# Performance work log

Measured on AMD Instinct MI355X. Metric: run time of the kernel, lower is better.

Reference implementation:

```python
import jax, jax.numpy as jnp
import numpy as np

B, S, H, DEPTH = 2, 2048, 8, 64
D_MODEL = H * DEPTH  # 512


def setup_inputs() -> dict:
    key = jax.random.key(0)
    ks = jax.random.split(key, 6)
    s = 0.02
    return {
        "emb_x": jax.random.normal(ks[0], (B, S, D_MODEL), dtype=jnp.float32),
        "pe_rel_t": jax.random.normal(ks[1], (B, S, D_MODEL), dtype=jnp.float32),
        "Wq": jax.random.normal(ks[2], (D_MODEL, D_MODEL), dtype=jnp.float32) * s,
        "bq": jnp.zeros((D_MODEL,), dtype=jnp.float32),
        "Wk": jax.random.normal(ks[3], (D_MODEL, D_MODEL), dtype=jnp.float32) * s,
        "bk": jnp.zeros((D_MODEL,), dtype=jnp.float32),
        "Wv": jax.random.normal(ks[4], (D_MODEL, D_MODEL), dtype=jnp.float32) * s,
        "bv": jnp.zeros((D_MODEL,), dtype=jnp.float32),
        "Wo": jax.random.normal(ks[5], (D_MODEL, D_MODEL), dtype=jnp.float32) * s,
        "bo": jnp.zeros((D_MODEL,), dtype=jnp.float32),
    }


def _split_heads(x):
    # [B, S, D_MODEL] -> [B, H, S, DEPTH]
    b, s, _ = x.shape
    return x.reshape(b, s, H, DEPTH).transpose(0, 2, 1, 3)


def reference(emb_x, pe_rel_t, Wq, bq, Wk, bk, Wv, bv, Wo, bo):
    # RPE attention: content and relative-position streams share WQ/WK.
    Q_c = _split_heads(emb_x @ Wq + bq)
    Q_r = _split_heads(pe_rel_t @ Wq + bq)
    K_c = _split_heads(emb_x @ Wk + bk)
    K_r = _split_heads(pe_rel_t @ Wk + bk)
    V_c = _split_heads(emb_x @ Wv + bv)

    logits = (
        jnp.einsum("bhqd,bhkd->bhqk", Q_c, K_c)
        + jnp.einsum("bhqd,bhkd->bhqk", Q_r, K_c)
        + jnp.einsum("bhqd,bhkd->bhqk", Q_c, K_r)
    ) / jnp.sqrt(jnp.asarray(DEPTH, dtype=emb_x.dtype))

    attn = jax.nn.softmax(logits, axis=-1)  # [B, H, S, S]
    z = jnp.einsum("bhqk,bhkd->bhqd", attn, V_c)  # [B, H, S, DEPTH]
    z = z.transpose(0, 2, 1, 3).reshape(emb_x.shape[0], -1, D_MODEL)
    out = z @ Wo + bo
    return out, attn
```

## Files before the change

### kernel.cpp

```cpp
#include <hip/hip_runtime.h>
#include <hip/hip_bf16.h>


typedef __bf16 bf16;
typedef bf16 bf16x4 __attribute__((ext_vector_type(4)));
typedef bf16 bf16x8 __attribute__((ext_vector_type(8)));
typedef float f32x4 __attribute__((ext_vector_type(4)));

#define B_ 2
#define S_ 2048
#define H_ 8
#define D_ 64
#define DM_ 512
#define M_ 4096

__global__ __launch_bounds__(256) void pack_x(const float4* __restrict__ emb,
                                              const float4* __restrict__ pe,
                                              bf16* __restrict__ xb,
                                              bf16* __restrict__ xp,
                                              bf16* __restrict__ xs) {
    int i = blockIdx.x * 256 + threadIdx.x;
    float4 a = emb[i], b = pe[i];
    int o = i * 4;
    bf16x4 va, vp, vs;
    va.x = (bf16)a.x; va.y = (bf16)a.y; va.z = (bf16)a.z; va.w = (bf16)a.w;
    vp.x = (bf16)b.x; vp.y = (bf16)b.y; vp.z = (bf16)b.z; vp.w = (bf16)b.w;
    vs.x = (bf16)(a.x + b.x); vs.y = (bf16)(a.y + b.y);
    vs.z = (bf16)(a.z + b.z); vs.w = (bf16)(a.w + b.w);
    *(bf16x4*)(xb + o) = va;
    *(bf16x4*)(xp + o) = vp;
    *(bf16x4*)(xs + o) = vs;
}

__global__ __launch_bounds__(256) void pack_w(const float* __restrict__ W,
                                              bf16* __restrict__ WT) {
    int idx = blockIdx.x * 256 + threadIdx.x;
    int n = idx >> 9, k = idx & 511;
    WT[idx] = (bf16)W[k * 512 + n];
}

template <int AMODE, int SMODE>
__global__ __launch_bounds__(256) void proj_gemm(const bf16* __restrict__ A,
                                                 const bf16* __restrict__ BT,
                                                 const float* __restrict__ bias,
                                                 float bscale,
                                                 void* __restrict__ Cout) {
    __shared__ bf16 As[64][72];
    __shared__ bf16 Bs[64][72];
    const int tid = threadIdx.x;
    const int lane = tid & 63;
    const int wave = tid >> 6;
    const int wm = wave >> 1, wn = wave & 1;
    const int row0 = blockIdx.x * 64;
    const int col0 = blockIdx.y * 64;
    const int lm = lane & 15, lk = (lane >> 4) * 8;

    f32x4 acc[2][2] = {{{0.f,0.f,0.f,0.f},{0.f,0.f,0.f,0.f}},
                       {{0.f,0.f,0.f,0.f},{0.f,0.f,0.f,0.f}}};

    for (int k0 = 0; k0 < 512; k0 += 64) {
        for (int i = 0; i < 2; ++i) {
            int idx = tid + i * 256;
            int r = idx >> 3, sg = (idx & 7) * 8;
            long aoff;
            int arow = row0 + r, acol = k0 + sg;
            if (AMODE == 0) {
                aoff = (long)arow * 512 + acol;
            } else {
                int b = arow >> 11, s = arow & 2047, h = acol >> 6, d = acol & 63;
                aoff = (((long)(b * H_ + h) * S_ + s) * 64) + d;
            }
            *(bf16x8*)&As[r][sg] = *(const bf16x8*)(A + aoff);
            *(bf16x8*)&Bs[r][sg] = *(const bf16x8*)(BT + (long)(col0 + r) * 512 + k0 + sg);
        }
        __syncthreads();
        for (int kk = 0; kk < 64; kk += 32) {
            bf16x8 af[2], bfr[2];
            for (int t = 0; t < 2; ++t) {
                af[t]  = *(const bf16x8*)&As[wm * 32 + t * 16 + lm][kk + lk];
                bfr[t] = *(const bf16x8*)&Bs[wn * 32 + t * 16 + lm][kk + lk];
            }
            for (int mt = 0; mt < 2; ++mt)
                for (int nt = 0; nt < 2; ++nt)
                    acc[mt][nt] = __builtin_amdgcn_mfma_f32_16x16x32_bf16(
                        af[mt], bfr[nt], acc[mt][nt], 0, 0, 0);
        }
        __syncthreads();
    }

    const int rbase = (lane >> 4) * 4;
    for (int mt = 0; mt < 2; ++mt)
        for (int nt = 0; nt < 2; ++nt)
            for (int r = 0; r < 4; ++r) {
                int row = row0 + wm * 32 + mt * 16 + rbase + r;
                int col = col0 + wn * 32 + nt * 16 + lm;
                float v = acc[mt][nt][r] + bias[col] * bscale;
                int b = row >> 11, s = row & 2047, h = col >> 6, d = col & 63;
                if (SMODE == 0) {
                    ((bf16*)Cout)[(((long)(b * H_ + h) * S_ + s) * 64) + d] = (bf16)v;
                } else if (SMODE == 1) {
                    ((bf16*)Cout)[(((long)(b * H_ + h) * 64 + d) * S_) + s] = (bf16)v;
                } else {
                    ((float*)Cout)[(long)row * 512 + col] = v;
                }
            }
}

__global__ __launch_bounds__(256) void attn_kernel(const bf16* __restrict__ Qc,
                                                   const bf16* __restrict__ Qr,
                                                   const bf16* __restrict__ Kc,
                                                   const bf16* __restrict__ Ks,
                                                   const bf16* __restrict__ Vt,
                                                   bf16* __restrict__ Zb,
                                                   float* __restrict__ attn_out) {
    __shared__ bf16 Kcs[64][72];
    __shared__ bf16 Kss[64][72];
    __shared__ bf16 Vts[64][72];
    __shared__ bf16 ptile[4][16][40];

    const int tid = threadIdx.x, lane = tid & 63, wave = tid >> 6;
    const int bh = blockIdx.x >> 5;
    const int qt = blockIdx.x & 31;
    const int qw = qt * 64 + wave * 16;
    const long kbase = (long)bh * (S_ * 64);
    const long vbase = (long)bh * (64 * S_);
    const int lm = lane & 15, lk = (lane >> 4) * 8;
    const float SC = 0.125f;

    bf16x8 qcf[2], qrf[2];
    for (int kt = 0; kt < 2; ++kt) {
        long off = kbase + (long)(qw + lm) * 64 + kt * 32 + lk;
        qcf[kt] = *(const bf16x8*)(Qc + off);
        qrf[kt] = *(const bf16x8*)(Qr + off);
    }

    float rsum[4] = {0.f, 0.f, 0.f, 0.f};
    f32x4 zacc[4] = {{0.f,0.f,0.f,0.f},{0.f,0.f,0.f,0.f},
                     {0.f,0.f,0.f,0.f},{0.f,0.f,0.f,0.f}};

    for (int key0 = 0; key0 < S_; key0 += 64) {
        __syncthreads();
        for (int i = 0; i < 2; ++i) {
            int idx = tid + i * 256, r = idx >> 3, sg = (idx & 7) * 8;
            *(bf16x8*)&Kcs[r][sg] = *(const bf16x8*)(Kc + kbase + (long)(key0 + r) * 64 + sg);
            *(bf16x8*)&Kss[r][sg] = *(const bf16x8*)(Ks + kbase + (long)(key0 + r) * 64 + sg);
            *(bf16x8*)&Vts[r][sg] = *(const bf16x8*)(Vt + vbase + (long)r * S_ + key0 + sg);
        }
        __syncthreads();
        for (int pair = 0; pair < 2; ++pair) {
            for (int nt = 0; nt < 2; ++nt) {
                const int keyl = pair * 32 + nt * 16;
                f32x4 acc = {0.f, 0.f, 0.f, 0.f};
                for (int kt = 0; kt < 2; ++kt) {
                    bf16x8 bs = *(const bf16x8*)&Kss[keyl + lm][kt * 32 + lk];
                    bf16x8 bc = *(const bf16x8*)&Kcs[keyl + lm][kt * 32 + lk];
                    acc = __builtin_amdgcn_mfma_f32_16x16x32_bf16(qcf[kt], bs, acc, 0, 0, 0);
                    acc = __builtin_amdgcn_mfma_f32_16x16x32_bf16(qrf[kt], bc, acc, 0, 0, 0);
                }
                for (int r = 0; r < 4; ++r) {
                    float p = __expf(acc[r] * SC);
                    rsum[r] += p;
                    ptile[wave][(lane >> 4) * 4 + r][nt * 16 + lm] = (bf16)p;
                }
            }
            __syncthreads();
            bf16x8 pa = *(const bf16x8*)&ptile[wave][lm][lk];
            for (int nt = 0; nt < 4; ++nt) {
                bf16x8 vb = *(const bf16x8*)&Vts[nt * 16 + lm][pair * 32 + lk];
                zacc[nt] = __builtin_amdgcn_mfma_f32_16x16x32_bf16(pa, vb, zacc[nt], 0, 0, 0);
            }
        }
    }

    float inv_r[4];
    for (int r = 0; r < 4; ++r) {
        float s = rsum[r];
        s += __shfl_xor(s, 1);
        s += __shfl_xor(s, 2);
        s += __shfl_xor(s, 4);
        s += __shfl_xor(s, 8);
        inv_r[r] = 1.0f / s;
    }

    for (int nt = 0; nt < 4; ++nt)
        for (int r = 0; r < 4; ++r)
            Zb[kbase + (long)(qw + (lane >> 4) * 4 + r) * 64 + nt * 16 + lm] =
                (bf16)(zacc[nt][r] * inv_r[r]);

    const long abase = (long)bh * S_ * S_;
    for (int key0 = 0; key0 < S_; key0 += 64) {
        __syncthreads();
        for (int i = 0; i < 2; ++i) {
            int idx = tid + i * 256, r = idx >> 3, sg = (idx & 7) * 8;
            *(bf16x8*)&Kcs[r][sg] = *(const bf16x8*)(Kc + kbase + (long)(key0 + r) * 64 + sg);
            *(bf16x8*)&Kss[r][sg] = *(const bf16x8*)(Ks + kbase + (long)(key0 + r) * 64 + sg);
        }
        __syncthreads();
        for (int nt = 0; nt < 4; ++nt) {
            const int keyl = nt * 16;
            f32x4 acc = {0.f, 0.f, 0.f, 0.f};
            for (int kt = 0; kt < 2; ++kt) {
                bf16x8 bs = *(const bf16x8*)&Kss[keyl + lm][kt * 32 + lk];
                bf16x8 bc = *(const bf16x8*)&Kcs[keyl + lm][kt * 32 + lk];
                acc = __builtin_amdgcn_mfma_f32_16x16x32_bf16(qcf[kt], bs, acc, 0, 0, 0);
                acc = __builtin_amdgcn_mfma_f32_16x16x32_bf16(qrf[kt], bc, acc, 0, 0, 0);
            }
            for (int r = 0; r < 4; ++r) {
                float p = __expf(acc[r] * SC) * inv_r[r];
                attn_out[abase + (long)(qw + (lane >> 4) * 4 + r) * S_ + key0 + keyl + lm] = p;
            }
        }
    }
}

extern "C" void kernel_launch(void* const* d_in, const int* in_sizes, int n_in,
                              void* d_out, int out_size, void* d_ws, size_t ws_size,
                              hipStream_t stream) {
    const float* emb = (const float*)d_in[0];
    const float* pe  = (const float*)d_in[1];
    const float* Wq  = (const float*)d_in[2];
    const float* bq  = (const float*)d_in[3];
    const float* Wk  = (const float*)d_in[4];
    const float* bk  = (const float*)d_in[5];
    const float* Wv  = (const float*)d_in[6];
    const float* bv  = (const float*)d_in[7];
    const float* Wo  = (const float*)d_in[8];
    const float* bo  = (const float*)d_in[9];

    float* outp = (float*)d_out;
    float* attn = outp + (long)B_ * S_ * DM_;

    char* w = (char*)d_ws;
    const long SZ_X = (long)M_ * DM_ * 2;
    const long SZ_W = (long)DM_ * DM_ * 2;
    bf16* Xb  = (bf16*)(w);
    bf16* Xp  = (bf16*)(w + SZ_X);
    bf16* Xs  = (bf16*)(w + 2 * SZ_X);
    bf16* WqT = (bf16*)(w + 3 * SZ_X);
    bf16* WkT = (bf16*)(w + 3 * SZ_X + SZ_W);
    bf16* WvT = (bf16*)(w + 3 * SZ_X + 2 * SZ_W);
    bf16* WoT = (bf16*)(w + 3 * SZ_X + 3 * SZ_W);
    char* p2  = w + 3 * SZ_X + 4 * SZ_W;
    bf16* Qc  = (bf16*)(p2);
    bf16* Qr  = (bf16*)(p2 + SZ_X);
    bf16* Kc  = (bf16*)(p2 + 2 * SZ_X);
    bf16* Ks  = (bf16*)(p2 + 3 * SZ_X);
    bf16* Vt  = (bf16*)(p2 + 4 * SZ_X);
    bf16* Zb  = (bf16*)(p2 + 5 * SZ_X);

    pack_x<<<(M_ * DM_ / 4) / 256, 256, 0, stream>>>(
        (const float4*)emb, (const float4*)pe, Xb, Xp, Xs);
    pack_w<<<(DM_ * DM_) / 256, 256, 0, stream>>>(Wq, WqT);
    pack_w<<<(DM_ * DM_) / 256, 256, 0, stream>>>(Wk, WkT);
    pack_w<<<(DM_ * DM_) / 256, 256, 0, stream>>>(Wv, WvT);
    pack_w<<<(DM_ * DM_) / 256, 256, 0, stream>>>(Wo, WoT);

    dim3 g(M_ / 64, DM_ / 64);
    proj_gemm<0, 0><<<g, 256, 0, stream>>>(Xb, WqT, bq, 1.f, Qc);
    proj_gemm<0, 0><<<g, 256, 0, stream>>>(Xp, WqT, bq, 1.f, Qr);
    proj_gemm<0, 0><<<g, 256, 0, stream>>>(Xb, WkT, bk, 1.f, Kc);
    proj_gemm<0, 0><<<g, 256, 0, stream>>>(Xs, WkT, bk, 2.f, Ks);
    proj_gemm<0, 1><<<g, 256, 0, stream>>>(Xb, WvT, bv, 1.f, Vt);

    attn_kernel<<<B_ * H_ * (S_ / 64), 256, 0, stream>>>(
        Qc, Qr, Kc, Ks, Vt, Zb, attn);

    proj_gemm<1, 2><<<g, 256, 0, stream>>>(Zb, WoT, bo, 1.f, (void*)outp);
}
```

Baseline: 429.9 us.

## Double-buffer attention K/V tiles, coalesce attn stores, batch weight packs and projections

The attention kernel now double-buffers Kc/Ks/Vt tiles in shared memory, prefetching the next tile into registers while computing the current one. It also removes the per-pair intra-block barrier and stores the fp32 attention matrix through an LDS staging buffer as float4 writes. The four weight transposes become one tiled kernel launch, and the five QKV projection GEMMs become one launch over a 40-column grid. Together these aim to cut global-memory latency stalls, uncoalesced writes of the large attention output, and launch overhead, at the cost of more shared memory and register pressure, which may reduce occupancy.

```diff
diff --git a/kernel.cpp b/kernel.cpp
--- a/kernel.cpp
+++ b/kernel.cpp
@@ -10,7 +10,6 @@
 #define B_ 2
 #define S_ 2048
 #define H_ 8
-#define D_ 64
 #define DM_ 512
 #define M_ 4096
 
@@ -32,24 +31,116 @@
     *(bf16x4*)(xs + o) = vs;
 }
 
-__global__ __launch_bounds__(256) void pack_w(const float* __restrict__ W,
-                                              bf16* __restrict__ WT) {
-    int idx = blockIdx.x * 256 + threadIdx.x;
-    int n = idx >> 9, k = idx & 511;
-    WT[idx] = (bf16)W[k * 512 + n];
-}
-
-template <int AMODE, int SMODE>
-__global__ __launch_bounds__(256) void proj_gemm(const bf16* __restrict__ A,
-                                                 const bf16* __restrict__ BT,
-                                                 const float* __restrict__ bias,
-                                                 float bscale,
-                                                 void* __restrict__ Cout) {
+__global__ __launch_bounds__(256) void pack_tw(
+    const float* __restrict__ W0, const float* __restrict__ W1,
+    const float* __restrict__ W2, const float* __restrict__ W3,
+    bf16* __restrict__ T0, bf16* __restrict__ T1,
+    bf16* __restrict__ T2, bf16* __restrict__ T3) {
+    __shared__ bf16 tile[64][66];
+    const float* W; bf16* T;
+    switch (blockIdx.z) {
+        case 0: W = W0; T = T0; break;
+        case 1: W = W1; T = T1; break;
+        case 2: W = W2; T = T2; break;
+        default: W = W3; T = T3; break;
+    }
+    const int tid = threadIdx.x;
+    const int r = tid >> 2, c = (tid & 3) * 16;
+    const int r0 = blockIdx.x * 64, c0 = blockIdx.y * 64;
+    for (int j = 0; j < 16; j += 4) {
+        float4 v = *(const float4*)&W[(long)(r0 + r) * 512 + c0 + c + j];
+        tile[r][c + j + 0] = (bf16)v.x; tile[r][c + j + 1] = (bf16)v.y;
+        tile[r][c + j + 2] = (bf16)v.z; tile[r][c + j + 3] = (bf16)v.w;
+    }
+    __syncthreads();
+    bf16x8 o0, o1;
+#pragma unroll
+    for (int j = 0; j < 8; ++j) { o0[j] = tile[c + j][r]; o1[j] = tile[c + 8 + j][r]; }
+    *(bf16x8*)&T[(long)(c0 + r) * 512 + r0 + c] = o0;
+    *(bf16x8*)&T[(long)(c0 + r) * 512 + r0 + c + 8] = o1;
+}
+
+__global__ __launch_bounds__(256) void proj5(
+    const bf16* __restrict__ Xb, const bf16* __restrict__ Xp, const bf16* __restrict__ Xs,
+    const bf16* __restrict__ WqT, const bf16* __restrict__ WkT, const bf16* __restrict__ WvT,
+    const float* __restrict__ bq, const float* __restrict__ bk, const float* __restrict__ bv,
+    bf16* __restrict__ Qc, bf16* __restrict__ Qr, bf16* __restrict__ Kc,
+    bf16* __restrict__ Ks, bf16* __restrict__ Vt) {
+    __shared__ bf16 As[64][72];
+    __shared__ bf16 Bs[64][72];
+    const int pj = blockIdx.y >> 3;
+    const int col0 = (blockIdx.y & 7) * 64;
+    const bf16* A; const bf16* BT; const float* bias; float bsc = 1.f;
+    bf16* out; int vmode = 0;
+    switch (pj) {
+        case 0: A = Xb; BT = WqT; bias = bq; out = Qc; break;
+        case 1: A = Xp; BT = WqT; bias = bq; out = Qr; break;
+        case 2: A = Xb; BT = WkT; bias = bk; out = Kc; break;
+        case 3: A = Xs; BT = WkT; bias = bk; bsc = 2.f; out = Ks; break;
+        default: A = Xb; BT = WvT; bias = bv; out = Vt; vmode = 1; break;
+    }
+    const int tid = threadIdx.x;
+    const int lane = tid & 63, wave = tid >> 6;
+    const int wm = wave >> 1, wn = wave & 1;
+    const int row0 = blockIdx.x * 64;
+    const int lm = lane & 15, lk = (lane >> 4) * 8;
+
+    f32x4 acc[2][2] = {{{0.f,0.f,0.f,0.f},{0.f,0.f,0.f,0.f}},
+                       {{0.f,0.f,0.f,0.f},{0.f,0.f,0.f,0.f}}};
+
+    for (int k0 = 0; k0 < 512; k0 += 64) {
+#pragma unroll
+        for (int i = 0; i < 2; ++i) {
+            int idx = tid + i * 256;
+            int r = idx >> 3, sg = (idx & 7) * 8;
+            *(bf16x8*)&As[r][sg] = *(const bf16x8*)(A + (long)(row0 + r) * 512 + k0 + sg);
+            *(bf16x8*)&Bs[r][sg] = *(const bf16x8*)(BT + (long)(col0 + r) * 512 + k0 + sg);
+        }
+        __syncthreads();
+#pragma unroll
+        for (int kk = 0; kk < 64; kk += 32) {
+            bf16x8 af[2], bfr[2];
+#pragma unroll
+            for (int t = 0; t < 2; ++t) {
+                af[t]  = *(const bf16x8*)&As[wm * 32 + t * 16 + lm][kk + lk];
+                bfr[t] = *(const bf16x8*)&Bs[wn * 32 + t * 16 + lm][kk + lk];
+            }
+#pragma unroll
+            for (int mt = 0; mt < 2; ++mt)
+#pragma unroll
+                for (int nt = 0; nt < 2; ++nt)
+                    acc[mt][nt] = __builtin_amdgcn_mfma_f32_16x16x32_bf16(
+                        af[mt], bfr[nt], acc[mt][nt], 0, 0, 0);
+        }
+        __syncthreads();
+    }
+
+    const int rbase = (lane >> 4) * 4;
+#pragma unroll
+    for (int mt = 0; mt < 2; ++mt)
+#pragma unroll
+        for (int nt = 0; nt < 2; ++nt)
+#pragma unroll
+            for (int r = 0; r < 4; ++r) {
+                int row = row0 + wm * 32 + mt * 16 + rbase + r;
+                int col = col0 + wn * 32 + nt * 16 + lm;
+                float v = acc[mt][nt][r] + bias[col] * bsc;
+                int b = row >> 11, s = row & 2047, h = col >> 6, d = col & 63;
+                if (vmode)
+                    out[(((long)(b * H_ + h) * 64 + d) * S_) + s] = (bf16)v;
+                else
+                    out[(((long)(b * H_ + h) * S_ + s) * 64) + d] = (bf16)v;
+            }
+}
+
+__global__ __launch_bounds__(256) void projO(const bf16* __restrict__ Zb,
+                                             const bf16* __restrict__ WoT,
+                                             const float* __restrict__ bo,
+                                             float* __restrict__ Cout) {
     __shared__ bf16 As[64][72];
     __shared__ bf16 Bs[64][72];
     const int tid = threadIdx.x;
-    const int lane = tid & 63;
-    const int wave = tid >> 6;
+    const int lane = tid & 63, wave = tid >> 6;
     const int wm = wave >> 1, wn = wave & 1;
     const int row0 = blockIdx.x * 64;
     const int col0 = blockIdx.y * 64;
@@ -59,28 +150,28 @@
                        {{0.f,0.f,0.f,0.f},{0.f,0.f,0.f,0.f}}};
 
     for (int k0 = 0; k0 < 512; k0 += 64) {
+#pragma unroll
         for (int i = 0; i < 2; ++i) {
             int idx = tid + i * 256;
             int r = idx >> 3, sg = (idx & 7) * 8;
-            long aoff;
             int arow = row0 + r, acol = k0 + sg;
-            if (AMODE == 0) {
-                aoff = (long)arow * 512 + acol;
-            } else {
-                int b = arow >> 11, s = arow & 2047, h = acol >> 6, d = acol & 63;
-                aoff = (((long)(b * H_ + h) * S_ + s) * 64) + d;
-            }
-            *(bf16x8*)&As[r][sg] = *(const bf16x8*)(A + aoff);
-            *(bf16x8*)&Bs[r][sg] = *(const bf16x8*)(BT + (long)(col0 + r) * 512 + k0 + sg);
-        }
-        __syncthreads();
+            int b = arow >> 11, s = arow & 2047, h = acol >> 6, d = acol & 63;
+            *(bf16x8*)&As[r][sg] =
+                *(const bf16x8*)(Zb + (((long)(b * H_ + h) * S_ + s) * 64) + d);
+            *(bf16x8*)&Bs[r][sg] = *(const bf16x8*)(WoT + (long)(col0 + r) * 512 + k0 + sg);
+        }
+        __syncthreads();
+#pragma unroll
         for (int kk = 0; kk < 64; kk += 32) {
             bf16x8 af[2], bfr[2];
+#pragma unroll
             for (int t = 0; t < 2; ++t) {
                 af[t]  = *(const bf16x8*)&As[wm * 32 + t * 16 + lm][kk + lk];
                 bfr[t] = *(const bf16x8*)&Bs[wn * 32 + t * 16 + lm][kk + lk];
             }
+#pragma unroll
             for (int mt = 0; mt < 2; ++mt)
+#pragma unroll
                 for (int nt = 0; nt < 2; ++nt)
                     acc[mt][nt] = __builtin_amdgcn_mfma_f32_16x16x32_bf16(
                         af[mt], bfr[nt], acc[mt][nt], 0, 0, 0);
@@ -89,20 +180,15 @@
     }
 
     const int rbase = (lane >> 4) * 4;
+#pragma unroll
     for (int mt = 0; mt < 2; ++mt)
+#pragma unroll
         for (int nt = 0; nt < 2; ++nt)
+#pragma unroll
             for (int r = 0; r < 4; ++r) {
                 int row = row0 + wm * 32 + mt * 16 + rbase + r;
                 int col = col0 + wn * 32 + nt * 16 + lm;
-                float v = acc[mt][nt][r] + bias[col] * bscale;
-                int b = row >> 11, s = row & 2047, h = col >> 6, d = col & 63;
-                if (SMODE == 0) {
-                    ((bf16*)Cout)[(((long)(b * H_ + h) * S_ + s) * 64) + d] = (bf16)v;
-                } else if (SMODE == 1) {
-                    ((bf16*)Cout)[(((long)(b * H_ + h) * 64 + d) * S_) + s] = (bf16)v;
-                } else {
-                    ((float*)Cout)[(long)row * 512 + col] = v;
-                }
+                Cout[(long)row * 512 + col] = acc[mt][nt][r] + bo[col];
             }
 }
 
@@ -113,10 +199,10 @@
                                                    const bf16* __restrict__ Vt,
                                                    bf16* __restrict__ Zb,
                                                    float* __restrict__ attn_out) {
-    __shared__ bf16 Kcs[64][72];
-    __shared__ bf16 Kss[64][72];
-    __shared__ bf16 Vts[64][72];
-    __shared__ bf16 ptile[4][16][40];
+    __shared__ bf16 Kcs[2][64][72];
+    __shared__ bf16 Kss[2][64][72];
+    __shared__ bf16 Vts[2][64][72];
+    __shared__ bf16 ptile[4][16][72];
 
     const int tid = threadIdx.x, lane = tid & 63, wave = tid >> 6;
     const int bh = blockIdx.x >> 5;
@@ -124,10 +210,11 @@
     const int qw = qt * 64 + wave * 16;
     const long kbase = (long)bh * (S_ * 64);
     const long vbase = (long)bh * (64 * S_);
-    const int lm = lane & 15, lk = (lane >> 4) * 8;
+    const int lm = lane & 15, lq = lane >> 4, lk = lq * 8;
     const float SC = 0.125f;
 
     bf16x8 qcf[2], qrf[2];
+#pragma unroll
     for (int kt = 0; kt < 2; ++kt) {
         long off = kbase + (long)(qw + lm) * 64 + kt * 32 + lk;
         qcf[kt] = *(const bf16x8*)(Qc + off);
@@ -138,41 +225,78 @@
     f32x4 zacc[4] = {{0.f,0.f,0.f,0.f},{0.f,0.f,0.f,0.f},
                      {0.f,0.f,0.f,0.f},{0.f,0.f,0.f,0.f}};
 
-    for (int key0 = 0; key0 < S_; key0 += 64) {
-        __syncthreads();
-        for (int i = 0; i < 2; ++i) {
-            int idx = tid + i * 256, r = idx >> 3, sg = (idx & 7) * 8;
-            *(bf16x8*)&Kcs[r][sg] = *(const bf16x8*)(Kc + kbase + (long)(key0 + r) * 64 + sg);
-            *(bf16x8*)&Kss[r][sg] = *(const bf16x8*)(Ks + kbase + (long)(key0 + r) * 64 + sg);
-            *(bf16x8*)&Vts[r][sg] = *(const bf16x8*)(Vt + vbase + (long)r * S_ + key0 + sg);
-        }
-        __syncthreads();
+#pragma unroll
+    for (int s = 0; s < 6; ++s) {
+        int idx = tid + s * 256;
+        int surf = idx >> 9, r = (idx >> 3) & 63, sg = (idx & 7) * 8;
+        bf16x8 v;
+        if (surf == 0)      v = *(const bf16x8*)(Kc + kbase + (long)r * 64 + sg);
+        else if (surf == 1) v = *(const bf16x8*)(Ks + kbase + (long)r * 64 + sg);
+        else                v = *(const bf16x8*)(Vt + vbase + (long)r * S_ + sg);
+        if (surf == 0)      *(bf16x8*)&Kcs[0][r][sg] = v;
+        else if (surf == 1) *(bf16x8*)&Kss[0][r][sg] = v;
+        else                *(bf16x8*)&Vts[0][r][sg] = v;
+    }
+    __syncthreads();
+
+    for (int t = 0; t < 32; ++t) {
+        const int p = t & 1;
+        const bool pf = (t + 1 < 32);
+        bf16x8 stg[6];
+        if (pf) {
+            const int kn = (t + 1) * 64;
+#pragma unroll
+            for (int s = 0; s < 6; ++s) {
+                int idx = tid + s * 256;
+                int surf = idx >> 9, r = (idx >> 3) & 63, sg = (idx & 7) * 8;
+                if (surf == 0)      stg[s] = *(const bf16x8*)(Kc + kbase + (long)(kn + r) * 64 + sg);
+                else if (surf == 1) stg[s] = *(const bf16x8*)(Ks + kbase + (long)(kn + r) * 64 + sg);
+                else                stg[s] = *(const bf16x8*)(Vt + vbase + (long)r * S_ + kn + sg);
+            }
+        }
+        f32x4 qk[4] = {{0.f,0.f,0.f,0.f},{0.f,0.f,0.f,0.f},
+                       {0.f,0.f,0.f,0.f},{0.f,0.f,0.f,0.f}};
+#pragma unroll
+        for (int nt = 0; nt < 4; ++nt)
+#pragma unroll
+            for (int kt = 0; kt < 2; ++kt) {
+                bf16x8 bs = *(const bf16x8*)&Kss[p][nt * 16 + lm][kt * 32 + lk];
+                bf16x8 bc = *(const bf16x8*)&Kcs[p][nt * 16 + lm][kt * 32 + lk];
+                qk[nt] = __builtin_amdgcn_mfma_f32_16x16x32_bf16(qcf[kt], bs, qk[nt], 0, 0, 0);
+                qk[nt] = __builtin_amdgcn_mfma_f32_16x16x32_bf16(qrf[kt], bc, qk[nt], 0, 0, 0);
+            }
+#pragma unroll
+        for (int nt = 0; nt < 4; ++nt)
+#pragma unroll
+            for (int r = 0; r < 4; ++r) {
+                float pv = __expf(qk[nt][r] * SC);
+                rsum[r] += pv;
+                ptile[wave][lq * 4 + r][nt * 16 + lm] = (bf16)pv;
+            }
+#pragma unroll
         for (int pair = 0; pair < 2; ++pair) {
-            for (int nt = 0; nt < 2; ++nt) {
-                const int keyl = pair * 32 + nt * 16;
-                f32x4 acc = {0.f, 0.f, 0.f, 0.f};
-                for (int kt = 0; kt < 2; ++kt) {
-                    bf16x8 bs = *(const bf16x8*)&Kss[keyl + lm][kt * 32 + lk];
-                    bf16x8 bc = *(const bf16x8*)&Kcs[keyl + lm][kt * 32 + lk];
-                    acc = __builtin_amdgcn_mfma_f32_16x16x32_bf16(qcf[kt], bs, acc, 0, 0, 0);
-                    acc = __builtin_amdgcn_mfma_f32_16x16x32_bf16(qrf[kt], bc, acc, 0, 0, 0);
-                }
-                for (int r = 0; r < 4; ++r) {
-                    float p = __expf(acc[r] * SC);
-                    rsum[r] += p;
-                    ptile[wave][(lane >> 4) * 4 + r][nt * 16 + lm] = (bf16)p;
-                }
-            }
-            __syncthreads();
-            bf16x8 pa = *(const bf16x8*)&ptile[wave][lm][lk];
+            bf16x8 pa = *(const bf16x8*)&ptile[wave][lm][pair * 32 + lk];
+#pragma unroll
             for (int nt = 0; nt < 4; ++nt) {
-                bf16x8 vb = *(const bf16x8*)&Vts[nt * 16 + lm][pair * 32 + lk];
+                bf16x8 vb = *(const bf16x8*)&Vts[p][nt * 16 + lm][pair * 32 + lk];
                 zacc[nt] = __builtin_amdgcn_mfma_f32_16x16x32_bf16(pa, vb, zacc[nt], 0, 0, 0);
             }
         }
+        if (pf) {
+#pragma unroll
+            for (int s = 0; s < 6; ++s) {
+                int idx = tid + s * 256;
+                int surf = idx >> 9, r = (idx >> 3) & 63, sg = (idx & 7) * 8;
+                if (surf == 0)      *(bf16x8*)&Kcs[p ^ 1][r][sg] = stg[s];
+                else if (surf == 1) *(bf16x8*)&Kss[p ^ 1][r][sg] = stg[s];
+                else                *(bf16x8*)&Vts[p ^ 1][r][sg] = stg[s];
+            }
+        }
+        __syncthreads();
     }
 
     float inv_r[4];
+#pragma unroll
     for (int r = 0; r < 4; ++r) {
         float s = rsum[r];
         s += __shfl_xor(s, 1);
@@ -182,34 +306,74 @@
         inv_r[r] = 1.0f / s;
     }
 
+#pragma unroll
     for (int nt = 0; nt < 4; ++nt)
+#pragma unroll
         for (int r = 0; r < 4; ++r)
-            Zb[kbase + (long)(qw + (lane >> 4) * 4 + r) * 64 + nt * 16 + lm] =
+            Zb[kbase + (long)(qw + lq * 4 + r) * 64 + nt * 16 + lm] =
                 (bf16)(zacc[nt][r] * inv_r[r]);
 
+    float* sbuf = (float*)&Vts[0][0][0];
+#pragma unroll
+    for (int s = 0; s < 4; ++s) {
+        int idx = tid + s * 256;
+        int surf = idx >> 9, r = (idx >> 3) & 63, sg = (idx & 7) * 8;
+        bf16x8 v = (surf == 0) ? *(const bf16x8*)(Kc + kbase + (long)r * 64 + sg)
+                               : *(const bf16x8*)(Ks + kbase + (long)r * 64 + sg);
+        if (surf == 0) *(bf16x8*)&Kcs[0][r][sg] = v;
+        else           *(bf16x8*)&Kss[0][r][sg] = v;
+    }
+    __syncthreads();
+
+    const int srow = lane >> 2, scol = (lane & 3) * 16;
     const long abase = (long)bh * S_ * S_;
-    for (int key0 = 0; key0 < S_; key0 += 64) {
-        __syncthreads();
-        for (int i = 0; i < 2; ++i) {
-            int idx = tid + i * 256, r = idx >> 3, sg = (idx & 7) * 8;
-            *(bf16x8*)&Kcs[r][sg] = *(const bf16x8*)(Kc + kbase + (long)(key0 + r) * 64 + sg);
-            *(bf16x8*)&Kss[r][sg] = *(const bf16x8*)(Ks + kbase + (long)(key0 + r) * 64 + sg);
-        }
-        __syncthreads();
-        for (int nt = 0; nt < 4; ++nt) {
-            const int keyl = nt * 16;
-            f32x4 acc = {0.f, 0.f, 0.f, 0.f};
+    for (int t = 0; t < 32; ++t) {
+        const int p = t & 1;
+        const int key0 = t * 64;
+        const bool pf = (t + 1 < 32);
+        bf16x8 stg[4];
+        if (pf) {
+            const int kn = key0 + 64;
+#pragma unroll
+            for (int s = 0; s < 4; ++s) {
+                int idx = tid + s * 256;
+                int surf = idx >> 9, r = (idx >> 3) & 63, sg = (idx & 7) * 8;
+                stg[s] = (surf == 0) ? *(const bf16x8*)(Kc + kbase + (long)(kn + r) * 64 + sg)
+                                     : *(const bf16x8*)(Ks + kbase + (long)(kn + r) * 64 + sg);
+            }
+        }
+        f32x4 qk[4] = {{0.f,0.f,0.f,0.f},{0.f,0.f,0.f,0.f},
+                       {0.f,0.f,0.f,0.f},{0.f,0.f,0.f,0.f}};
+#pragma unroll
+        for (int nt = 0; nt < 4; ++nt)
+#pragma unroll
             for (int kt = 0; kt < 2; ++kt) {
-                bf16x8 bs = *(const bf16x8*)&Kss[keyl + lm][kt * 32 + lk];
-                bf16x8 bc = *(const bf16x8*)&Kcs[keyl + lm][kt * 32 + lk];
-                acc = __builtin_amdgcn_mfma_f32_16x16x32_bf16(qcf[kt], bs, acc, 0, 0, 0);
-                acc = __builtin_amdgcn_mfma_f32_16x16x32_bf16(qrf[kt], bc, acc, 0, 0, 0);
-            }
-            for (int r = 0; r < 4; ++r) {
-                float p = __expf(acc[r] * SC) * inv_r[r];
-                attn_out[abase + (long)(qw + (lane >> 4) * 4 + r) * S_ + key0 + keyl + lm] = p;
-            }
-        }
+                bf16x8 bs = *(const bf16x8*)&Kss[p][nt * 16 + lm][kt * 32 + lk];
+                bf16x8 bc = *(const bf16x8*)&Kcs[p][nt * 16 + lm][kt * 32 + lk];
+                qk[nt] = __builtin_amdgcn_mfma_f32_16x16x32_bf16(qcf[kt], bs, qk[nt], 0, 0, 0);
+                qk[nt] = __builtin_amdgcn_mfma_f32_16x16x32_bf16(qrf[kt], bc, qk[nt], 0, 0, 0);
+            }
+#pragma unroll
+        for (int nt = 0; nt < 4; ++nt)
+#pragma unroll
+            for (int r = 0; r < 4; ++r)
+                sbuf[((wave * 16) + lq * 4 + r) * 72 + nt * 16 + lm] =
+                    __expf(qk[nt][r] * SC) * inv_r[r];
+#pragma unroll
+        for (int j = 0; j < 4; ++j) {
+            f32x4 v = *(const f32x4*)&sbuf[((wave * 16) + srow) * 72 + scol + j * 4];
+            *(f32x4*)&attn_out[abase + (long)(qw + srow) * S_ + key0 + scol + j * 4] = v;
+        }
+        if (pf) {
+#pragma unroll
+            for (int s = 0; s < 4; ++s) {
+                int idx = tid + s * 256;
+                int surf = idx >> 9, r = (idx >> 3) & 63, sg = (idx & 7) * 8;
+                if (surf == 0) *(bf16x8*)&Kcs[p ^ 1][r][sg] = stg[s];
+                else           *(bf16x8*)&Kss[p ^ 1][r][sg] = stg[s];
+            }
+        }
+        __syncthreads();
     }
 }
 
@@ -250,20 +414,13 @@
 
     pack_x<<<(M_ * DM_ / 4) / 256, 256, 0, stream>>>(
         (const float4*)emb, (const float4*)pe, Xb, Xp, Xs);
-    pack_w<<<(DM_ * DM_) / 256, 256, 0, stream>>>(Wq, WqT);
-    pack_w<<<(DM_ * DM_) / 256, 256, 0, stream>>>(Wk, WkT);
-    pack_w<<<(DM_ * DM_) / 256, 256, 0, stream>>>(Wv, WvT);
-    pack_w<<<(DM_ * DM_) / 256, 256, 0, stream>>>(Wo, WoT);
-
-    dim3 g(M_ / 64, DM_ / 64);
-    proj_gemm<0, 0><<<g, 256, 0, stream>>>(Xb, WqT, bq, 1.f, Qc);
-    proj_gemm<0, 0><<<g, 256, 0, stream>>>(Xp, WqT, bq, 1.f, Qr);
-    proj_gemm<0, 0><<<g, 256, 0, stream>>>(Xb, WkT, bk, 1.f, Kc);
-    proj_gemm<0, 0><<<g, 256, 0, stream>>>(Xs, WkT, bk, 2.f, Ks);
-    proj_gemm<0, 1><<<g, 256, 0, stream>>>(Xb, WvT, bv, 1.f, Vt);
+    pack_tw<<<dim3(8, 8, 4), 256, 0, stream>>>(Wq, Wk, Wv, Wo, WqT, WkT, WvT, WoT);
+
+    proj5<<<dim3(M_ / 64, 40), 256, 0, stream>>>(
+        Xb, Xp, Xs, WqT, WkT, WvT, bq, bk, bv, Qc, Qr, Kc, Ks, Vt);
 
     attn_kernel<<<B_ * H_ * (S_ / 64), 256, 0, stream>>>(
         Qc, Qr, Kc, Ks, Vt, Zb, attn);
 
-    proj_gemm<1, 2><<<g, 256, 0, stream>>>(Zb, WoT, bo, 1.f, (void*)outp);
-}
+    projO<<<dim3(M_ / 64, DM_ / 64), 256, 0, stream>>>(Zb, WoT, bo, outp);
+}
```

After: 439.2 us. +2.2%, slower.
